# Kernel tuning notes

Hardware: AMD Instinct MI355X
Metric: run time of the kernel (lower is better)

The kernel has to match this reference:

```python
import jax, jax.numpy as jnp
import numpy as np
import itertools

LN_EPS = 1e-5

def _combo_idx(d):
    # lexicographic (i<j) and (i<j<k) combination indices, matching the torch nested loops
    pairs = np.array(list(itertools.combinations(range(d), 2)), dtype=np.int32)  # [P,2]
    trips = np.array(list(itertools.combinations(range(d), 3)), dtype=np.int32)  # [T,3]
    return pairs, trips

def setup_inputs() -> dict:
    key = jax.random.key(0)
    k1, k2 = jax.random.split(key)
    d, batch, out_dim = 64, 4096, 512
    total = d + d * (d - 1) // 2 + d * (d - 1) * (d - 2) // 6  # 63744
    x = jax.random.normal(k1, (batch, d), dtype=jnp.float32)
    W = jax.random.normal(k2, (total, out_dim), dtype=jnp.float32) * (1.0 / np.sqrt(total))
    b = jnp.zeros((out_dim,), dtype=jnp.float32)
    gamma = jnp.ones((out_dim,), dtype=jnp.float32)
    beta = jnp.zeros((out_dim,), dtype=jnp.float32)
    return {"x": x, "W": W, "b": b, "gamma": gamma, "beta": beta}

def reference(x, W, b, gamma, beta):
    d = x.shape[1]
    pairs, trips = _combo_idx(d)  # static numpy index tables
    # pairwise products x_i * x_j for i<j  -> [B, C(d,2)]
    pw = x[:, pairs[:, 0]] * x[:, pairs[:, 1]]
    # triplet products x_i * x_j * x_k for i<j<k -> [B, C(d,3)]
    tp = x[:, trips[:, 0]] * x[:, trips[:, 1]] * x[:, trips[:, 2]]
    feats = jnp.concatenate([x, pw, tp], axis=1)  # [B, total]
    h = feats @ W + b  # Linear
    # LayerNorm over last dim
    mu = jnp.mean(h, axis=-1, keepdims=True)
    var = jnp.var(h, axis=-1, keepdims=True)
    hn = (h - mu) * jax.lax.rsqrt(var + LN_EPS) * gamma + beta
    return jax.nn.relu(hn)
```

## Files before the change

### kernel.cpp

```cpp
#include <hip/hip_runtime.h>
#include <stdint.h>

#define D 64
#define KTOT 43744
#define NPAIR 2016
#define NOUT 512
#define MROWS 4096
#define BM 128
#define BN 256
#define BK 64
#define NSTEPS ((KTOT + BK - 1) / BK)
#define KPAD (NSTEPS * BK)
#define K2B (KPAD * 2)

typedef __attribute__((ext_vector_type(8))) short short8;
typedef __attribute__((ext_vector_type(4))) float f32x4;
typedef __attribute__((ext_vector_type(4))) uint32_t u32x4;

__device__ __forceinline__ uint32_t cvtpk(float lo, float hi) {
  uint32_t r;
  asm("v_cvt_pk_bf16_f32 %0, %1, %2" : "=v"(r) : "v"(lo), "v"(hi));
  return r;
}

__device__ __forceinline__ void load_b128_to_lds(const void* gsrc, void* ldst) {
  typedef const __attribute__((address_space(1))) uint32_t* GP;
  typedef __attribute__((address_space(3))) uint32_t* LP;
  __builtin_amdgcn_global_load_lds((GP)(uintptr_t)gsrc, (LP)(uintptr_t)ldst, 16, 0, 0);
}

__device__ __forceinline__ void unrank(int k, int& i, int& j, int& l) {
  if (k < D) {
    i = k; j = D; l = D;
  } else if (k < D + NPAIR) {
    int p = k - D;
    i = 0;
    while (p >= D - 1 - i) { p -= D - 1 - i; ++i; }
    j = i + 1 + p; l = D;
  } else {
    int t = k - (D + NPAIR);
    i = 0;
    for (;;) { int c = (D - 1 - i) * (D - 2 - i) / 2; if (t < c) break; t -= c; ++i; }
    j = i + 1;
    while (t >= D - 1 - j) { t -= D - 1 - j; ++j; }
    l = j + 1 + t;
  }
}

__device__ __forceinline__ bool inc_idx(int& i, int& j, int& l) {
  if (l >= D) {
    if (j >= D) { ++i; if (i == D) { i = 0; j = 1; } return true; }
    ++j;
    if (j == D) { ++i; j = i + 1; if (j == D) { i = 0; j = 1; l = 2; } }
    return true;
  }
  ++l;
  if (l == D) {
    ++j; l = j + 1;
    if (l == D) { ++i; j = i + 1; l = j + 1; }
    return true;
  }
  return false;
}

__global__ void build_idx_k(uint32_t* __restrict__ idx) {
  int k = blockIdx.x * 256 + threadIdx.x;
  if (k >= KPAD) return;
  if (k >= KTOT) { idx[k] = 64u | (64u << 8) | (64u << 16); return; }
  int i, j, l;
  unrank(k, i, j, l);
  idx[k] = (uint32_t)i | ((uint32_t)j << 8) | ((uint32_t)l << 16);
}

__global__ void wtrans_k(const float* __restrict__ W, char* __restrict__ Wt) {
  __shared__ float tile[64][65];
  int bk = blockIdx.x;
  int bn = blockIdx.y;
  int t = threadIdx.x;
  int k0 = bk * 64, n0 = bn * 64;
  int col = t & 63, r0 = t >> 6;
  #pragma unroll
  for (int p = 0; p < 16; ++p) {
    int row = p * 4 + r0;
    tile[col][row] = (k0 + row < KTOT) ? W[(size_t)(k0 + row) * NOUT + (n0 + col)] : 0.0f;
  }
  __syncthreads();
  for (int u = t; u < 512; u += 256) {
    int n = u >> 3, s = u & 7;
    int ng = n0 + n;
    u32x4 v = {cvtpk(tile[n][s * 8 + 0], tile[n][s * 8 + 1]),
               cvtpk(tile[n][s * 8 + 2], tile[n][s * 8 + 3]),
               cvtpk(tile[n][s * 8 + 4], tile[n][s * 8 + 5]),
               cvtpk(tile[n][s * 8 + 6], tile[n][s * 8 + 7])};
    int sp = s ^ (ng & 7);
    *(u32x4*)(Wt + (size_t)ng * K2B + (size_t)k0 * 2 + (sp << 4)) = v;
  }
}

template<int USE_WT, int USE_IDX>
__global__ void __launch_bounds__(512, 4)
gemm_k(const float* __restrict__ x, const float* __restrict__ W,
       const char* __restrict__ Wt, const uint32_t* __restrict__ idxg,
       float* __restrict__ part, int S, int Slog, int steps_per) {
  __shared__ float XmT[D * 128];
  __shared__ __align__(16) char Al[BM * 128];
  __shared__ __align__(16) char Bl[BN * 128];

  const int t = threadIdx.x;
  const int lane = t & 63;
  const int w = t >> 6;

  const int mb = blockIdx.x & 31;
  const int ns = blockIdx.x >> 5;
  const int nb = ns >> Slog;
  const int sb = ns & (S - 1);

  {
    int m = t >> 2, i0 = (t & 3) * 16;
    const float* src = x + (size_t)(mb * BM + m) * D + i0;
    #pragma unroll
    for (int c = 0; c < 4; ++c) {
      f32x4 v = *(const f32x4*)(src + c * 4);
      #pragma unroll
      for (int e = 0; e < 4; ++e) XmT[(i0 + c * 4 + e) * 128 + m] = v[e];
    }
  }
  __syncthreads();

  f32x4 acc[4][4];
  #pragma unroll
  for (int a = 0; a < 4; ++a)
    #pragma unroll
    for (int b = 0; b < 4; ++b) {
      f32x4 z = {0.f, 0.f, 0.f, 0.f};
      acc[a][b] = z;
    }

  const int wr = w >> 2, wc = w & 3;
  const int g = lane >> 4;

  int Abase[4], Bbase[4];
  #pragma unroll
  for (int fm = 0; fm < 4; ++fm) {
    int m = wr * 64 + fm * 16 + (lane & 15);
    Abase[fm] = m * 128 + ((g ^ (m & 7)) << 4);
  }
  #pragma unroll
  for (int fn = 0; fn < 4; ++fn) {
    int n = wc * 64 + fn * 16 + (lane & 15);
    Bbase[fn] = n * 128 + ((g ^ (n & 7)) << 4);
  }

  uint32_t BrowOff[4];
  #pragma unroll
  for (int inst = 0; inst < 4; ++inst) {
    int row = nb * BN + w * 32 + inst * 8 + (lane >> 3);
    BrowOff[inst] = (uint32_t)row * K2B + ((lane & 7) << 4);
  }

  const int fg_m = t & 127;
  const int fg_kh = t >> 7;
  const float* xcol = XmT + fg_m;
  const uint32_t Awr0 = (uint32_t)(fg_m * 128 + (((fg_kh * 2 + 0) ^ (fg_m & 7)) << 4));
  const uint32_t Awr1 = (uint32_t)(fg_m * 128 + (((fg_kh * 2 + 1) ^ (fg_m & 7)) << 4));

  const int ks0 = sb * steps_per;
  const int ks1 = (ks0 + steps_per < NSTEPS) ? (ks0 + steps_per) : NSTEPS;

  for (int ks = ks0; ks < ks1; ++ks) {
    const int k0 = ks * BK;

    if (USE_WT) {
      #pragma unroll
      for (int inst = 0; inst < 4; ++inst)
        load_b128_to_lds(Wt + BrowOff[inst] + (uint32_t)k0 * 2,
                         Bl + w * 4096 + inst * 1024);
    }

    {
      uint32_t pk[8];
      const int kbase = k0 + fg_kh * 16;
      if (USE_IDX) {
        u32x4 I[4];
        const u32x4* ip = (const u32x4*)(idxg + kbase);
        #pragma unroll
        for (int c = 0; c < 4; ++c) I[c] = ip[c];

        if (kbase >= D + NPAIR) {
          uint32_t prev = 0xFFFFFFFFu;
          float pp = 0.0f;
          #pragma unroll
          for (int c = 0; c < 4; ++c) {
            float fv[4];
            #pragma unroll
            for (int e = 0; e < 4; ++e) {
              uint32_t uu = I[c][e];
              uint32_t ij = uu & 0xFFFFu;
              if (ij != prev) {
                pp = xcol[(uu & 63u) * 128] * xcol[((uu >> 8) & 63u) * 128];
                prev = ij;
              }
              fv[e] = pp * xcol[((uu >> 16) & 63u) * 128];
            }
            pk[c * 2 + 0] = cvtpk(fv[0], fv[1]);
            pk[c * 2 + 1] = cvtpk(fv[2], fv[3]);
          }
        } else {
          #pragma unroll
          for (int c = 0; c < 4; ++c) {
            float fv[4];
            #pragma unroll
            for (int e = 0; e < 4; ++e) {
              uint32_t uu = I[c][e];
              uint32_t ji = (uu >> 8) & 0xFFu, li = uu >> 16;
              float xi = xcol[(uu & 63u) * 128];
              float xj = (ji < 64u) ? xcol[(ji & 63u) * 128] : 1.0f;
              float xl = (li < 64u) ? xcol[(li & 63u) * 128] : 1.0f;
              fv[e] = xi * xj * xl;
            }
            pk[c * 2 + 0] = cvtpk(fv[0], fv[1]);
            pk[c * 2 + 1] = cvtpk(fv[2], fv[3]);
          }
        }
      } else {
        int ii, jj, ll;
        unrank(kbase < KTOT ? kbase : KTOT - 1, ii, jj, ll);
        float fv[16];
        #pragma unroll
        for (int h = 0; h < 16; ++h) {
          float xi = xcol[(ii & 63) * 128];
          float xj = (jj < 64) ? xcol[(jj & 63) * 128] : 1.0f;
          float xl = (ll < 64) ? xcol[(ll & 63) * 128] : 1.0f;
          fv[h] = (kbase + h < KTOT) ? xi * xj * xl : 0.0f;
          if (h < 15) inc_idx(ii, jj, ll);
        }
        #pragma unroll
        for (int c = 0; c < 8; ++c) pk[c] = cvtpk(fv[2 * c], fv[2 * c + 1]);
      }
      u32x4 v0 = {pk[0], pk[1], pk[2], pk[3]};
      u32x4 v1 = {pk[4], pk[5], pk[6], pk[7]};
      *(u32x4*)(Al + Awr0) = v0;
      *(u32x4*)(Al + Awr1) = v1;
    }

    if (!USE_WT) {
      #pragma unroll
      for (int i2 = 0; i2 < 4; ++i2) {
        int u = t + i2 * 512;
        int n = u & 255, s = u >> 8;
        const float* wp = W + (size_t)(k0 + s * 8) * NOUT + nb * BN + n;
        float f[8];
        #pragma unroll
        for (int e = 0; e < 8; ++e)
          f[e] = (k0 + s * 8 + e < KTOT) ? wp[(size_t)e * NOUT] : 0.0f;
        u32x4 v = {cvtpk(f[0], f[1]), cvtpk(f[2], f[3]),
                   cvtpk(f[4], f[5]), cvtpk(f[6], f[7])};
        *(u32x4*)(Bl + n * 128 + ((s ^ (n & 7)) << 4)) = v;
      }
    }

    __syncthreads();

    #pragma unroll
    for (int kc = 0; kc < 2; ++kc) {
      short8 av[4], bv[4];
      #pragma unroll
      for (int fm = 0; fm < 4; ++fm)
        av[fm] = *(const short8*)(Al + (Abase[fm] ^ (kc << 6)));
      #pragma unroll
      for (int fn = 0; fn < 4; ++fn)
        bv[fn] = *(const short8*)(Bl + (Bbase[fn] ^ (kc << 6)));
      #pragma unroll
      for (int fm = 0; fm < 4; ++fm)
        #pragma unroll
        for (int fn = 0; fn < 4; ++fn)
          acc[fm][fn] = __builtin_amdgcn_mfma_f32_16x16x32_bf16(av[fm], bv[fn], acc[fm][fn], 0, 0, 0);
    }
    __syncthreads();
  }

  #pragma unroll
  for (int fm = 0; fm < 4; ++fm) {
    int rbase = mb * BM + wr * 64 + fm * 16 + ((lane >> 4) << 2);
    #pragma unroll
    for (int fn = 0; fn < 4; ++fn) {
      int col = nb * BN + wc * 64 + fn * 16 + (lane & 15);
      float* dst = part + ((size_t)sb * MROWS + rbase) * NOUT + col;
      #pragma unroll
      for (int r = 0; r < 4; ++r) dst[(size_t)r * NOUT] = acc[fm][fn][r];
    }
  }
}

__global__ void ln_k(const float* part, int S,
                     const float* __restrict__ bias, const float* __restrict__ gamma,
                     const float* __restrict__ beta, float* out) {
  int row = blockIdx.x;
  int t = threadIdx.x;
  float v[2];
  #pragma unroll
  for (int q = 0; q < 2; ++q) {
    int c = t + q * 256;
    float s = bias[c];
    for (int sbi = 0; sbi < S; ++sbi)
      s += part[((size_t)sbi * MROWS + row) * NOUT + c];
    v[q] = s;
  }
  float sum = v[0] + v[1];
  float sq = v[0] * v[0] + v[1] * v[1];
  #pragma unroll
  for (int off = 32; off > 0; off >>= 1) {
    sum += __shfl_xor(sum, off, 64);
    sq  += __shfl_xor(sq, off, 64);
  }
  __shared__ float red[8];
  int wv = t >> 6;
  if ((t & 63) == 0) { red[wv] = sum; red[4 + wv] = sq; }
  __syncthreads();
  sum = red[0] + red[1] + red[2] + red[3];
  sq  = red[4] + red[5] + red[6] + red[7];
  float mu = sum * (1.0f / NOUT);
  float var = sq * (1.0f / NOUT) - mu * mu;
  float rs = rsqrtf(var + 1e-5f);
  #pragma unroll
  for (int q = 0; q < 2; ++q) {
    int c = t + q * 256;
    float hn = (v[q] - mu) * rs * gamma[c] + beta[c];
    out[(size_t)row * NOUT + c] = fmaxf(hn, 0.0f);
  }
}

extern "C" void kernel_launch(void* const* d_in, const int* in_sizes, int n_in,
                              void* d_out, int out_size, void* d_ws, size_t ws_size,
                              hipStream_t stream) {
  const float* x     = (const float*)d_in[0];
  const float* W     = (const float*)d_in[1];
  const float* bias  = (const float*)d_in[2];
  const float* gamma = (const float*)d_in[3];
  const float* beta  = (const float*)d_in[4];
  float* out = (float*)d_out;
  (void)in_sizes; (void)n_in; (void)out_size;

  const size_t IDXB = 262144;
  const size_t WTB  = (size_t)NOUT * K2B;
  const size_t PART = (size_t)MROWS * NOUT * sizeof(float);

  char* base = (char*)d_ws;
  uint32_t* idx = (uint32_t*)base;
  char* Wt = base + IDXB;

  const bool has_idx = ws_size >= IDXB;
  bool use_wt = false;
  int S = 1, Slog = 0;
  if (ws_size >= IDXB + WTB + 8 * PART)      { use_wt = true;  S = 8; Slog = 3; }
  else if (ws_size >= IDXB + 8 * PART)       { use_wt = false; S = 8; Slog = 3; }
  else if (ws_size >= IDXB + WTB + 4 * PART) { use_wt = true;  S = 4; Slog = 2; }
  else if (ws_size >= IDXB + 4 * PART)       { use_wt = false; S = 4; Slog = 2; }
  else if (ws_size >= IDXB + WTB + 2 * PART) { use_wt = true;  S = 2; Slog = 1; }
  else if (ws_size >= IDXB + 2 * PART)       { use_wt = false; S = 2; Slog = 1; }
  else if (ws_size >= IDXB + WTB)            { use_wt = true;  S = 1; Slog = 0; }

  float* part = out;
  if (S > 1) part = (float*)(base + IDXB + (use_wt ? WTB : 0));

  int steps_per = (NSTEPS + S - 1) / S;
  int grid = 32 * (NOUT / BN) * S;

  if (has_idx) build_idx_k<<<KPAD / 256, 256, 0, stream>>>(idx);
  if (use_wt)  wtrans_k<<<dim3(NSTEPS, 8), 256, 0, stream>>>(W, Wt);

  if (use_wt)
    gemm_k<1, 1><<<grid, 512, 0, stream>>>(x, W, Wt, idx, part, S, Slog, steps_per);
  else if (has_idx)
    gemm_k<0, 1><<<grid, 512, 0, stream>>>(x, W, Wt, idx, part, S, Slog, steps_per);
  else
    gemm_k<0, 0><<<grid, 512, 0, stream>>>(x, W, Wt, nullptr, part, S, Slog, steps_per);

  ln_k<<<MROWS, 256, 0, stream>>>(part, S, bias, gamma, beta, out);
}
```

Before: 271.8 us.

## Widen GEMM tile to full output width so features are built once per row block

```diff
diff --git a/kernel.cpp b/kernel.cpp
--- a/kernel.cpp
+++ b/kernel.cpp
@@ -7,7 +7,7 @@
 #define NOUT 512
 #define MROWS 4096
 #define BM 128
-#define BN 256
+#define BN 512
 #define BK 64
 #define NSTEPS ((KTOT + BK - 1) / BK)
 #define KPAD (NSTEPS * BK)
@@ -98,10 +98,10 @@
 }
 
 template<int USE_WT, int USE_IDX>
-__global__ void __launch_bounds__(512, 4)
+__global__ void __launch_bounds__(512, 2)
 gemm_k(const float* __restrict__ x, const float* __restrict__ W,
        const char* __restrict__ Wt, const uint32_t* __restrict__ idxg,
-       float* __restrict__ part, int S, int Slog, int steps_per) {
+       float* __restrict__ part, int S, int steps_per) {
   __shared__ float XmT[D * 128];
   __shared__ __align__(16) char Al[BM * 128];
   __shared__ __align__(16) char Bl[BN * 128];
@@ -111,9 +111,7 @@
   const int w = t >> 6;
 
   const int mb = blockIdx.x & 31;
-  const int ns = blockIdx.x >> 5;
-  const int nb = ns >> Slog;
-  const int sb = ns & (S - 1);
+  const int sb = blockIdx.x >> 5;
 
   {
     int m = t >> 2, i0 = (t & 3) * 16;
@@ -127,11 +125,11 @@
   }
   __syncthreads();
 
-  f32x4 acc[4][4];
+  f32x4 acc[4][8];
   #pragma unroll
   for (int a = 0; a < 4; ++a)
     #pragma unroll
-    for (int b = 0; b < 4; ++b) {
+    for (int b = 0; b < 8; ++b) {
       f32x4 z = {0.f, 0.f, 0.f, 0.f};
       acc[a][b] = z;
     }
@@ -139,22 +137,22 @@
   const int wr = w >> 2, wc = w & 3;
   const int g = lane >> 4;
 
-  int Abase[4], Bbase[4];
+  int Abase[4], Bbase[8];
   #pragma unroll
   for (int fm = 0; fm < 4; ++fm) {
     int m = wr * 64 + fm * 16 + (lane & 15);
     Abase[fm] = m * 128 + ((g ^ (m & 7)) << 4);
   }
   #pragma unroll
-  for (int fn = 0; fn < 4; ++fn) {
-    int n = wc * 64 + fn * 16 + (lane & 15);
+  for (int fn = 0; fn < 8; ++fn) {
+    int n = wc * 128 + fn * 16 + (lane & 15);
     Bbase[fn] = n * 128 + ((g ^ (n & 7)) << 4);
   }
 
-  uint32_t BrowOff[4];
-  #pragma unroll
-  for (int inst = 0; inst < 4; ++inst) {
-    int row = nb * BN + w * 32 + inst * 8 + (lane >> 3);
+  uint32_t BrowOff[8];
+  #pragma unroll
+  for (int inst = 0; inst < 8; ++inst) {
+    int row = w * 64 + inst * 8 + (lane >> 3);
     BrowOff[inst] = (uint32_t)row * K2B + ((lane & 7) << 4);
   }
 
@@ -172,21 +170,17 @@
 
     if (USE_WT) {
       #pragma unroll
-      for (int inst = 0; inst < 4; ++inst)
+      for (int inst = 0; inst < 8; ++inst)
         load_b128_to_lds(Wt + BrowOff[inst] + (uint32_t)k0 * 2,
-                         Bl + w * 4096 + inst * 1024);
+                         Bl + w * 8192 + inst * 1024);
     }
 
     {
       uint32_t pk[8];
       const int kbase = k0 + fg_kh * 16;
       if (USE_IDX) {
-        u32x4 I[4];
-        const u32x4* ip = (const u32x4*)(idxg + kbase);
-        #pragma unroll
-        for (int c = 0; c < 4; ++c) I[c] = ip[c];
-
         if (kbase >= D + NPAIR) {
+          const uint32_t* ip = idxg + kbase;
           uint32_t prev = 0xFFFFFFFFu;
           float pp = 0.0f;
           #pragma unroll
@@ -194,7 +188,7 @@
             float fv[4];
             #pragma unroll
             for (int e = 0; e < 4; ++e) {
-              uint32_t uu = I[c][e];
+              uint32_t uu = __builtin_amdgcn_readfirstlane(ip[c * 4 + e]);
               uint32_t ij = uu & 0xFFFFu;
               if (ij != prev) {
                 pp = xcol[(uu & 63u) * 128] * xcol[((uu >> 8) & 63u) * 128];
@@ -206,12 +200,14 @@
             pk[c * 2 + 1] = cvtpk(fv[2], fv[3]);
           }
         } else {
+          const u32x4* ip = (const u32x4*)(idxg + kbase);
           #pragma unroll
           for (int c = 0; c < 4; ++c) {
+            u32x4 I = ip[c];
             float fv[4];
             #pragma unroll
             for (int e = 0; e < 4; ++e) {
-              uint32_t uu = I[c][e];
+              uint32_t uu = I[e];
               uint32_t ji = (uu >> 8) & 0xFFu, li = uu >> 16;
               float xi = xcol[(uu & 63u) * 128];
               float xj = (ji < 64u) ? xcol[(ji & 63u) * 128] : 1.0f;
@@ -245,10 +241,10 @@
 
     if (!USE_WT) {
       #pragma unroll
-      for (int i2 = 0; i2 < 4; ++i2) {
+      for (int i2 = 0; i2 < 8; ++i2) {
         int u = t + i2 * 512;
-        int n = u & 255, s = u >> 8;
-        const float* wp = W + (size_t)(k0 + s * 8) * NOUT + nb * BN + n;
+        int n = u & 511, s = u >> 9;
+        const float* wp = W + (size_t)(k0 + s * 8) * NOUT + n;
         float f[8];
         #pragma unroll
         for (int e = 0; e < 8; ++e)
@@ -261,21 +257,22 @@
 
     __syncthreads();
 
+    __builtin_amdgcn_s_setprio(1);
     #pragma unroll
     for (int kc = 0; kc < 2; ++kc) {
-      short8 av[4], bv[4];
+      short8 av[4];
       #pragma unroll
       for (int fm = 0; fm < 4; ++fm)
         av[fm] = *(const short8*)(Al + (Abase[fm] ^ (kc << 6)));
       #pragma unroll
-      for (int fn = 0; fn < 4; ++fn)
-        bv[fn] = *(const short8*)(Bl + (Bbase[fn] ^ (kc << 6)));
-      #pragma unroll
-      for (int fm = 0; fm < 4; ++fm)
+      for (int fn = 0; fn < 8; ++fn) {
+        short8 bv = *(const short8*)(Bl + (Bbase[fn] ^ (kc << 6)));
         #pragma unroll
-        for (int fn = 0; fn < 4; ++fn)
-          acc[fm][fn] = __builtin_amdgcn_mfma_f32_16x16x32_bf16(av[fm], bv[fn], acc[fm][fn], 0, 0, 0);
-    }
+        for (int fm = 0; fm < 4; ++fm)
+          acc[fm][fn] = __builtin_amdgcn_mfma_f32_16x16x32_bf16(av[fm], bv, acc[fm][fn], 0, 0, 0);
+      }
+    }
+    __builtin_amdgcn_s_setprio(0);
     __syncthreads();
   }
 
@@ -283,8 +280,8 @@
   for (int fm = 0; fm < 4; ++fm) {
     int rbase = mb * BM + wr * 64 + fm * 16 + ((lane >> 4) << 2);
     #pragma unroll
-    for (int fn = 0; fn < 4; ++fn) {
-      int col = nb * BN + wc * 64 + fn * 16 + (lane & 15);
+    for (int fn = 0; fn < 8; ++fn) {
+      int col = wc * 128 + fn * 16 + (lane & 15);
       float* dst = part + ((size_t)sb * MROWS + rbase) * NOUT + col;
       #pragma unroll
       for (int r = 0; r < 4; ++r) dst[(size_t)r * NOUT] = acc[fm][fn][r];
@@ -351,30 +348,30 @@
 
   const bool has_idx = ws_size >= IDXB;
   bool use_wt = false;
-  int S = 1, Slog = 0;
-  if (ws_size >= IDXB + WTB + 8 * PART)      { use_wt = true;  S = 8; Slog = 3; }
-  else if (ws_size >= IDXB + 8 * PART)       { use_wt = false; S = 8; Slog = 3; }
-  else if (ws_size >= IDXB + WTB + 4 * PART) { use_wt = true;  S = 4; Slog = 2; }
-  else if (ws_size >= IDXB + 4 * PART)       { use_wt = false; S = 4; Slog = 2; }
-  else if (ws_size >= IDXB + WTB + 2 * PART) { use_wt = true;  S = 2; Slog = 1; }
-  else if (ws_size >= IDXB + 2 * PART)       { use_wt = false; S = 2; Slog = 1; }
-  else if (ws_size >= IDXB + WTB)            { use_wt = true;  S = 1; Slog = 0; }
+  int S = 1;
+  if (ws_size >= IDXB + WTB + 8 * PART)      { use_wt = true;  S = 8; }
+  else if (ws_size >= IDXB + 8 * PART)       { use_wt = false; S = 8; }
+  else if (ws_size >= IDXB + WTB + 4 * PART) { use_wt = true;  S = 4; }
+  else if (ws_size >= IDXB + 4 * PART)       { use_wt = false; S = 4; }
+  else if (ws_size >= IDXB + WTB + 2 * PART) { use_wt = true;  S = 2; }
+  else if (ws_size >= IDXB + 2 * PART)       { use_wt = false; S = 2; }
+  else if (ws_size >= IDXB + WTB)            { use_wt = true;  S = 1; }
 
   float* part = out;
   if (S > 1) part = (float*)(base + IDXB + (use_wt ? WTB : 0));
 
   int steps_per = (NSTEPS + S - 1) / S;
-  int grid = 32 * (NOUT / BN) * S;
+  int grid = 32 * S;
 
   if (has_idx) build_idx_k<<<KPAD / 256, 256, 0, stream>>>(idx);
   if (use_wt)  wtrans_k<<<dim3(NSTEPS, 8), 256, 0, stream>>>(W, Wt);
 
   if (use_wt)
-    gemm_k<1, 1><<<grid, 512, 0, stream>>>(x, W, Wt, idx, part, S, Slog, steps_per);
+    gemm_k<1, 1><<<grid, 512, 0, stream>>>(x, W, Wt, idx, part, S, steps_per);
   else if (has_idx)
-    gemm_k<0, 1><<<grid, 512, 0, stream>>>(x, W, Wt, idx, part, S, Slog, steps_per);
+    gemm_k<0, 1><<<grid, 512, 0, stream>>>(x, W, Wt, idx, part, S, steps_per);
   else
-    gemm_k<0, 0><<<grid, 512, 0, stream>>>(x, W, Wt, nullptr, part, S, Slog, steps_per);
+    gemm_k<0, 0><<<grid, 512, 0, stream>>>(x, W, Wt, nullptr, part, S, steps_per);
 
   ln_k<<<MROWS, 256, 0, stream>>>(part, S, bias, gamma, beta, out);
 }
```

After: 327.6 us. 20.5% more time.

## Double-buffer GEMM LDS stages with BK=32 and add XCD-aware block swizzle

Applied to the files above, without the earlier changes.

```diff
diff --git a/kernel.cpp b/kernel.cpp
--- a/kernel.cpp
+++ b/kernel.cpp
@@ -8,10 +8,9 @@
 #define MROWS 4096
 #define BM 128
 #define BN 256
-#define BK 64
-#define NSTEPS ((KTOT + BK - 1) / BK)
-#define KPAD (NSTEPS * BK)
-#define K2B (KPAD * 2)
+#define BK 32
+#define NSTEPS (KTOT / BK)
+#define K2B (KTOT * 2)
 
 typedef __attribute__((ext_vector_type(8))) short short8;
 typedef __attribute__((ext_vector_type(4))) float f32x4;
@@ -65,8 +64,7 @@
 
 __global__ void build_idx_k(uint32_t* __restrict__ idx) {
   int k = blockIdx.x * 256 + threadIdx.x;
-  if (k >= KPAD) return;
-  if (k >= KTOT) { idx[k] = 64u | (64u << 8) | (64u << 16); return; }
+  if (k >= KTOT) return;
   int i, j, l;
   unrank(k, i, j, l);
   idx[k] = (uint32_t)i | ((uint32_t)j << 8) | ((uint32_t)l << 16);
@@ -86,14 +84,18 @@
   }
   __syncthreads();
   for (int u = t; u < 512; u += 256) {
-    int n = u >> 3, s = u & 7;
+    int n = u >> 3, s8 = u & 7;
+    int chunk = s8 >> 2, s = s8 & 3;
+    int kc0 = k0 + chunk * 32;
+    if (kc0 >= KTOT) continue;
     int ng = n0 + n;
-    u32x4 v = {cvtpk(tile[n][s * 8 + 0], tile[n][s * 8 + 1]),
-               cvtpk(tile[n][s * 8 + 2], tile[n][s * 8 + 3]),
-               cvtpk(tile[n][s * 8 + 4], tile[n][s * 8 + 5]),
-               cvtpk(tile[n][s * 8 + 6], tile[n][s * 8 + 7])};
-    int sp = s ^ (ng & 7);
-    *(u32x4*)(Wt + (size_t)ng * K2B + (size_t)k0 * 2 + (sp << 4)) = v;
+    int b = chunk * 32 + s * 8;
+    u32x4 v = {cvtpk(tile[n][b + 0], tile[n][b + 1]),
+               cvtpk(tile[n][b + 2], tile[n][b + 3]),
+               cvtpk(tile[n][b + 4], tile[n][b + 5]),
+               cvtpk(tile[n][b + 6], tile[n][b + 7])};
+    int sp = s ^ (ng & 3);
+    *(u32x4*)(Wt + (size_t)ng * K2B + (size_t)kc0 * 2 + (sp << 4)) = v;
   }
 }
 
@@ -101,17 +103,25 @@
 __global__ void __launch_bounds__(512, 4)
 gemm_k(const float* __restrict__ x, const float* __restrict__ W,
        const char* __restrict__ Wt, const uint32_t* __restrict__ idxg,
-       float* __restrict__ part, int S, int Slog, int steps_per) {
+       float* __restrict__ part, int S, int Slog, int steps_per, int swz) {
   __shared__ float XmT[D * 128];
-  __shared__ __align__(16) char Al[BM * 128];
-  __shared__ __align__(16) char Bl[BN * 128];
+  __shared__ __align__(16) char Al[2][BM * 64];
+  __shared__ __align__(16) char Bl[2][BN * 64];
 
   const int t = threadIdx.x;
   const int lane = t & 63;
   const int w = t >> 6;
 
-  const int mb = blockIdx.x & 31;
-  const int ns = blockIdx.x >> 5;
+  int mb, ns;
+  if (swz) {
+    int xcd = blockIdx.x & 7;
+    int sub = blockIdx.x >> 3;
+    ns = xcd + 8 * (sub >> 5);
+    mb = sub & 31;
+  } else {
+    mb = blockIdx.x & 31;
+    ns = blockIdx.x >> 5;
+  }
   const int nb = ns >> Slog;
   const int sb = ns & (S - 1);
 
@@ -125,7 +135,6 @@
       for (int e = 0; e < 4; ++e) XmT[(i0 + c * 4 + e) * 128 + m] = v[e];
     }
   }
-  __syncthreads();
 
   f32x4 acc[4][4];
   #pragma unroll
@@ -143,140 +152,135 @@
   #pragma unroll
   for (int fm = 0; fm < 4; ++fm) {
     int m = wr * 64 + fm * 16 + (lane & 15);
-    Abase[fm] = m * 128 + ((g ^ (m & 7)) << 4);
+    Abase[fm] = m * 64 + ((g ^ (m & 3)) << 4);
   }
   #pragma unroll
   for (int fn = 0; fn < 4; ++fn) {
     int n = wc * 64 + fn * 16 + (lane & 15);
-    Bbase[fn] = n * 128 + ((g ^ (n & 7)) << 4);
-  }
-
-  uint32_t BrowOff[4];
-  #pragma unroll
-  for (int inst = 0; inst < 4; ++inst) {
-    int row = nb * BN + w * 32 + inst * 8 + (lane >> 3);
-    BrowOff[inst] = (uint32_t)row * K2B + ((lane & 7) << 4);
+    Bbase[fn] = n * 64 + ((g ^ (n & 3)) << 4);
+  }
+
+  uint32_t BrowOff[2];
+  #pragma unroll
+  for (int inst = 0; inst < 2; ++inst) {
+    int row = nb * BN + w * 32 + inst * 16 + (lane >> 2);
+    BrowOff[inst] = (uint32_t)row * K2B + ((lane & 3) << 4);
   }
 
   const int fg_m = t & 127;
   const int fg_kh = t >> 7;
   const float* xcol = XmT + fg_m;
-  const uint32_t Awr0 = (uint32_t)(fg_m * 128 + (((fg_kh * 2 + 0) ^ (fg_m & 7)) << 4));
-  const uint32_t Awr1 = (uint32_t)(fg_m * 128 + (((fg_kh * 2 + 1) ^ (fg_m & 7)) << 4));
+  const uint32_t Awr = (uint32_t)(fg_m * 64 + ((fg_kh ^ (fg_m & 3)) << 4));
 
   const int ks0 = sb * steps_per;
   const int ks1 = (ks0 + steps_per < NSTEPS) ? (ks0 + steps_per) : NSTEPS;
 
-  for (int ks = ks0; ks < ks1; ++ks) {
+  __syncthreads();
+
+  auto do_stage = [&](int ks, int buf) {
     const int k0 = ks * BK;
-
     if (USE_WT) {
       #pragma unroll
-      for (int inst = 0; inst < 4; ++inst)
+      for (int inst = 0; inst < 2; ++inst)
         load_b128_to_lds(Wt + BrowOff[inst] + (uint32_t)k0 * 2,
-                         Bl + w * 4096 + inst * 1024);
-    }
-
+                         &Bl[buf][w * 2048 + inst * 1024]);
+    }
     {
-      uint32_t pk[8];
-      const int kbase = k0 + fg_kh * 16;
+      uint32_t pk[4];
+      const int kbase = k0 + fg_kh * 8;
       if (USE_IDX) {
-        u32x4 I[4];
-        const u32x4* ip = (const u32x4*)(idxg + kbase);
-        #pragma unroll
-        for (int c = 0; c < 4; ++c) I[c] = ip[c];
-
         if (kbase >= D + NPAIR) {
+          const u32x4* ip = (const u32x4*)(idxg + kbase);
+          u32x4 I0 = ip[0], I1 = ip[1];
           uint32_t prev = 0xFFFFFFFFu;
           float pp = 0.0f;
+          float fv[8];
           #pragma unroll
-          for (int c = 0; c < 4; ++c) {
-            float fv[4];
-            #pragma unroll
-            for (int e = 0; e < 4; ++e) {
-              uint32_t uu = I[c][e];
-              uint32_t ij = uu & 0xFFFFu;
-              if (ij != prev) {
-                pp = xcol[(uu & 63u) * 128] * xcol[((uu >> 8) & 63u) * 128];
-                prev = ij;
-              }
-              fv[e] = pp * xcol[((uu >> 16) & 63u) * 128];
+          for (int e = 0; e < 8; ++e) {
+            uint32_t uu = __builtin_amdgcn_readfirstlane(e < 4 ? I0[e & 3] : I1[e & 3]);
+            uint32_t ij = uu & 0xFFFFu;
+            if (ij != prev) {
+              pp = xcol[(uu & 63u) * 128] * xcol[((uu >> 8) & 63u) * 128];
+              prev = ij;
             }
-            pk[c * 2 + 0] = cvtpk(fv[0], fv[1]);
-            pk[c * 2 + 1] = cvtpk(fv[2], fv[3]);
+            fv[e] = pp * xcol[((uu >> 16) & 63u) * 128];
           }
+          #pragma unroll
+          for (int c = 0; c < 4; ++c) pk[c] = cvtpk(fv[2 * c], fv[2 * c + 1]);
         } else {
+          const u32x4* ip = (const u32x4*)(idxg + kbase);
+          u32x4 I0 = ip[0], I1 = ip[1];
+          float fv[8];
           #pragma unroll
-          for (int c = 0; c < 4; ++c) {
-            float fv[4];
-            #pragma unroll
-            for (int e = 0; e < 4; ++e) {
-              uint32_t uu = I[c][e];
-              uint32_t ji = (uu >> 8) & 0xFFu, li = uu >> 16;
-              float xi = xcol[(uu & 63u) * 128];
-              float xj = (ji < 64u) ? xcol[(ji & 63u) * 128] : 1.0f;
-              float xl = (li < 64u) ? xcol[(li & 63u) * 128] : 1.0f;
-              fv[e] = xi * xj * xl;
-            }
-            pk[c * 2 + 0] = cvtpk(fv[0], fv[1]);
-            pk[c * 2 + 1] = cvtpk(fv[2], fv[3]);
+          for (int e = 0; e < 8; ++e) {
+            uint32_t uu = (e < 4) ? I0[e & 3] : I1[e & 3];
+            uint32_t ji = (uu >> 8) & 0xFFu, li = uu >> 16;
+            float xi = xcol[(uu & 63u) * 128];
+            float xj = (ji < 64u) ? xcol[(ji & 63u) * 128] : 1.0f;
+            float xl = (li < 64u) ? xcol[(li & 63u) * 128] : 1.0f;
+            fv[e] = xi * xj * xl;
           }
+          #pragma unroll
+          for (int c = 0; c < 4; ++c) pk[c] = cvtpk(fv[2 * c], fv[2 * c + 1]);
         }
       } else {
         int ii, jj, ll;
-        unrank(kbase < KTOT ? kbase : KTOT - 1, ii, jj, ll);
-        float fv[16];
+        unrank(kbase, ii, jj, ll);
+        float fv[8];
         #pragma unroll
-        for (int h = 0; h < 16; ++h) {
+        for (int h = 0; h < 8; ++h) {
           float xi = xcol[(ii & 63) * 128];
           float xj = (jj < 64) ? xcol[(jj & 63) * 128] : 1.0f;
           float xl = (ll < 64) ? xcol[(ll & 63) * 128] : 1.0f;
-          fv[h] = (kbase + h < KTOT) ? xi * xj * xl : 0.0f;
-          if (h < 15) inc_idx(ii, jj, ll);
+          fv[h] = xi * xj * xl;
+          if (h < 7) inc_idx(ii, jj, ll);
         }
         #pragma unroll
-        for (int c = 0; c < 8; ++c) pk[c] = cvtpk(fv[2 * c], fv[2 * c + 1]);
+        for (int c = 0; c < 4; ++c) pk[c] = cvtpk(fv[2 * c], fv[2 * c + 1]);
       }
       u32x4 v0 = {pk[0], pk[1], pk[2], pk[3]};
-      u32x4 v1 = {pk[4], pk[5], pk[6], pk[7]};
-      *(u32x4*)(Al + Awr0) = v0;
-      *(u32x4*)(Al + Awr1) = v1;
-    }
-
+      *(u32x4*)(&Al[buf][0] + Awr) = v0;
+    }
     if (!USE_WT) {
       #pragma unroll
-      for (int i2 = 0; i2 < 4; ++i2) {
+      for (int i2 = 0; i2 < 2; ++i2) {
         int u = t + i2 * 512;
         int n = u & 255, s = u >> 8;
         const float* wp = W + (size_t)(k0 + s * 8) * NOUT + nb * BN + n;
         float f[8];
         #pragma unroll
-        for (int e = 0; e < 8; ++e)
-          f[e] = (k0 + s * 8 + e < KTOT) ? wp[(size_t)e * NOUT] : 0.0f;
+        for (int e = 0; e < 8; ++e) f[e] = wp[(size_t)e * NOUT];
         u32x4 v = {cvtpk(f[0], f[1]), cvtpk(f[2], f[3]),
                    cvtpk(f[4], f[5]), cvtpk(f[6], f[7])};
-        *(u32x4*)(Bl + n * 128 + ((s ^ (n & 7)) << 4)) = v;
+        *(u32x4*)(&Bl[buf][0] + n * 64 + ((s ^ (n & 3)) << 4)) = v;
       }
     }
-
-    __syncthreads();
-
-    #pragma unroll
-    for (int kc = 0; kc < 2; ++kc) {
-      short8 av[4], bv[4];
-      #pragma unroll
-      for (int fm = 0; fm < 4; ++fm)
-        av[fm] = *(const short8*)(Al + (Abase[fm] ^ (kc << 6)));
+  };
+
+  do_stage(ks0, 0);
+  __syncthreads();
+
+  int cur = 0;
+  for (int ks = ks0; ks < ks1; ++ks) {
+    if (ks + 1 < ks1) do_stage(ks + 1, cur ^ 1);
+
+    __builtin_amdgcn_s_setprio(1);
+    short8 av[4], bv[4];
+    #pragma unroll
+    for (int fm = 0; fm < 4; ++fm)
+      av[fm] = *(const short8*)(&Al[cur][0] + Abase[fm]);
+    #pragma unroll
+    for (int fn = 0; fn < 4; ++fn)
+      bv[fn] = *(const short8*)(&Bl[cur][0] + Bbase[fn]);
+    #pragma unroll
+    for (int fm = 0; fm < 4; ++fm)
       #pragma unroll
       for (int fn = 0; fn < 4; ++fn)
-        bv[fn] = *(const short8*)(Bl + (Bbase[fn] ^ (kc << 6)));
-      #pragma unroll
-      for (int fm = 0; fm < 4; ++fm)
-        #pragma unroll
-        for (int fn = 0; fn < 4; ++fn)
-          acc[fm][fn] = __builtin_amdgcn_mfma_f32_16x16x32_bf16(av[fm], bv[fn], acc[fm][fn], 0, 0, 0);
-    }
-    __syncthreads();
+        acc[fm][fn] = __builtin_amdgcn_mfma_f32_16x16x32_bf16(av[fm], bv[fn], acc[fm][fn], 0, 0, 0);
+    __builtin_amdgcn_s_setprio(0);
+
+    if (ks + 1 < ks1) __syncthreads();
+    cur ^= 1;
   }
 
   #pragma unroll
@@ -365,16 +369,17 @@
 
   int steps_per = (NSTEPS + S - 1) / S;
   int grid = 32 * (NOUT / BN) * S;
-
-  if (has_idx) build_idx_k<<<KPAD / 256, 256, 0, stream>>>(idx);
-  if (use_wt)  wtrans_k<<<dim3(NSTEPS, 8), 256, 0, stream>>>(W, Wt);
+  int swz = (grid == 512) ? 1 : 0;
+
+  if (has_idx) build_idx_k<<<(KTOT + 255) / 256, 256, 0, stream>>>(idx);
+  if (use_wt)  wtrans_k<<<dim3((KTOT + 63) / 64, 8), 256, 0, stream>>>(W, Wt);
 
   if (use_wt)
-    gemm_k<1, 1><<<grid, 512, 0, stream>>>(x, W, Wt, idx, part, S, Slog, steps_per);
+    gemm_k<1, 1><<<grid, 512, 0, stream>>>(x, W, Wt, idx, part, S, Slog, steps_per, swz);
   else if (has_idx)
-    gemm_k<0, 1><<<grid, 512, 0, stream>>>(x, W, Wt, idx, part, S, Slog, steps_per);
+    gemm_k<0, 1><<<grid, 512, 0, stream>>>(x, W, Wt, idx, part, S, Slog, steps_per, swz);
   else
-    gemm_k<0, 0><<<grid, 512, 0, stream>>>(x, W, Wt, nullptr, part, S, Slog, steps_per);
+    gemm_k<0, 0><<<grid, 512, 0, stream>>>(x, W, Wt, nullptr, part, S, Slog, steps_per, swz);
 
   ln_k<<<MROWS, 256, 0, stream>>>(part, S, bias, gamma, beta, out);
 }
```

Result: slower. 314.9 us (+15.8%).
